# Optimization experiments

Measured on AMD Instinct MI355X. Metric: run time of the kernel, lower is better.

## Reference

```python
import jax, jax.numpy as jnp
import numpy as np

D_MODEL = 1024
NUM_HEAD = 16
D_K = D_MODEL // NUM_HEAD
FFN_D = 4096
EPS = 1e-5


def _layernorm(x, gamma, beta):
    mu = jnp.mean(x, axis=-1, keepdims=True)
    var = jnp.mean(jnp.square(x - mu), axis=-1, keepdims=True)
    return (x - mu) * jax.lax.rsqrt(var + EPS) * gamma + beta


def setup_inputs() -> dict:
    key = jax.random.key(0)
    ks = jax.random.split(key, 16)
    s = 1.0 / np.sqrt(D_MODEL)
    sf = 1.0 / np.sqrt(FFN_D)
    # weights stored as [in, out] (transpose of torch nn.Linear.weight)
    return {
        "x": jax.random.normal(ks[0], (4, 2048, D_MODEL), dtype=jnp.float32),
        "wq": jax.random.uniform(ks[1], (D_MODEL, D_MODEL), jnp.float32, -s, s),
        "bq": jax.random.uniform(ks[2], (D_MODEL,), jnp.float32, -s, s),
        "wk": jax.random.uniform(ks[3], (D_MODEL, D_MODEL), jnp.float32, -s, s),
        "bk": jax.random.uniform(ks[4], (D_MODEL,), jnp.float32, -s, s),
        "wv": jax.random.uniform(ks[5], (D_MODEL, D_MODEL), jnp.float32, -s, s),
        "bv": jax.random.uniform(ks[6], (D_MODEL,), jnp.float32, -s, s),
        "wo": jax.random.uniform(ks[7], (D_MODEL, D_MODEL), jnp.float32, -s, s),
        "bo": jax.random.uniform(ks[8], (D_MODEL,), jnp.float32, -s, s),
        "w1": jax.random.uniform(ks[9], (D_MODEL, FFN_D), jnp.float32, -s, s),
        "b1": jax.random.uniform(ks[10], (FFN_D,), jnp.float32, -s, s),
        "w2": jax.random.uniform(ks[11], (FFN_D, D_MODEL), jnp.float32, -sf, sf),
        "b2": jax.random.uniform(ks[12], (D_MODEL,), jnp.float32, -sf, sf),
        "g1": jnp.ones((D_MODEL,), jnp.float32),
        "be1": jnp.zeros((D_MODEL,), jnp.float32),
        "g2": jnp.ones((D_MODEL,), jnp.float32),
        "be2": jnp.zeros((D_MODEL,), jnp.float32),
    }


def reference(x, wq, bq, wk, bk, wv, bv, wo, bo, w1, b1, w2, b2, g1, be1, g2, be2):
    B, S, _ = x.shape
    resid1 = x
    # project and split heads: [B, H, S, d_k]
    def heads(w, b):
        return (x @ w + b).reshape(B, S, NUM_HEAD, D_K).transpose(0, 2, 1, 3)
    q = heads(wq, bq)
    k = heads(wk, bk)
    v = heads(wv, bv)
    scores = jnp.einsum("bhsd,bhtd->bhst", q, k) / jnp.sqrt(jnp.float32(D_K))
    attn = jax.nn.softmax(scores, axis=-1)
    ctx = jnp.einsum("bhst,bhtd->bhsd", attn, v)
    ctx = ctx.transpose(0, 2, 1, 3).reshape(B, S, D_MODEL)
    attn_out = ctx @ wo + bo
    x1 = _layernorm(resid1 + attn_out, g1, be1)
    ffn = jax.nn.relu(x1 @ w1 + b1) @ w2 + b2
    return _layernorm(x1 + ffn, g2, be2)
```

## Files before the change

### kernel.cpp

```cpp
#include <hip/hip_runtime.h>

typedef unsigned short u16;
typedef __attribute__((ext_vector_type(8))) u16 u16x8;
typedef __attribute__((ext_vector_type(8))) __bf16 bf16x8;
typedef __attribute__((ext_vector_type(4))) float floatx4;
typedef __attribute__((ext_vector_type(16))) float floatx16;
typedef __attribute__((ext_vector_type(4))) unsigned int u32x4;

#define MFMA16(a, b, c) __builtin_amdgcn_mfma_f32_16x16x32_bf16( \
    __builtin_bit_cast(bf16x8, a), __builtin_bit_cast(bf16x8, b), c, 0, 0, 0)
#define MFMA32(a, b, c) __builtin_amdgcn_mfma_f32_32x32x16_bf16( \
    __builtin_bit_cast(bf16x8, a), __builtin_bit_cast(bf16x8, b), c, 0, 0, 0)

#if __has_builtin(__builtin_amdgcn_exp2f)
#define EXP2(x) __builtin_amdgcn_exp2f(x)
#else
#define EXP2(x) exp2f(x)
#endif

__device__ __forceinline__ float bf2f(u16 h) {
  unsigned u = ((unsigned)h) << 16;
  float f;
  __builtin_memcpy(&f, &u, 4);
  return f;
}
__device__ __forceinline__ u16 f2bf(float f) {
  unsigned u;
  __builtin_memcpy(&u, &f, 4);
  u += 0x7fff + ((u >> 16) & 1);
  return (u16)(u >> 16);
}

__device__ __forceinline__ unsigned cvt_pk_bf16(float a, float b) {
  unsigned r;
  asm("v_cvt_pk_bf16_f32 %0, %1, %2" : "=v"(r) : "v"(a), "v"(b));
  return r;
}
__device__ __forceinline__ void pl32_swap(unsigned& a, unsigned& b) {
  asm("v_permlane32_swap_b32 %0, %1" : "+v"(a), "+v"(b));
}

typedef __attribute__((address_space(1))) const unsigned int gas_u32;
typedef __attribute__((address_space(3))) unsigned int las_u32;

__device__ __forceinline__ void gld_lds16(const u16* g, u16* l) {
  __builtin_amdgcn_global_load_lds((gas_u32*)g, (las_u32*)l, 16, 0, 0);
}

__global__ __launch_bounds__(256) void transpose_k(const float* __restrict__ in,
                                                   u16* __restrict__ out, int R, int C) {
  __shared__ u16 tile[64][65];
  int c0 = blockIdx.x * 64, r0 = blockIdx.y * 64;
  int tc = threadIdx.x & 63, tr = threadIdx.x >> 6;
#pragma unroll
  for (int i = 0; i < 16; ++i)
    tile[tr + i * 4][tc] = f2bf(in[(size_t)(r0 + tr + i * 4) * C + c0 + tc]);
  __syncthreads();
#pragma unroll
  for (int i = 0; i < 16; ++i)
    out[(size_t)(c0 + tr + i * 4) * R + r0 + tc] = tile[tc][tr + i * 4];
}

__global__ __launch_bounds__(256) void convert_k(const float* __restrict__ in,
                                                 u16* __restrict__ out) {
  size_t idx = ((size_t)blockIdx.x * 256 + threadIdx.x) * 8;
  floatx4 f0 = *(const floatx4*)(in + idx);
  floatx4 f1 = *(const floatx4*)(in + idx + 4);
  u16x8 o;
#pragma unroll
  for (int e = 0; e < 4; ++e) o[e] = f2bf(f0[e]);
#pragma unroll
  for (int e = 0; e < 4; ++e) o[4 + e] = f2bf(f1[e]);
  *(u16x8*)(out + idx) = o;
}

template <bool C_F32, bool BIAS_ROW>
__global__ __launch_bounds__(256, 2) void gemm_bt(const u16* __restrict__ A,
                                                  const u16* __restrict__ BT,
                                                  const float* __restrict__ bias,
                                                  void* __restrict__ Cv, int M, int N, int K,
                                                  int relu) {
  __shared__ __align__(16) u16 As[2][128 * 64];
  __shared__ __align__(16) u16 Bs[2][128 * 64];
  const int tid = threadIdx.x, lane = tid & 63, wave = tid >> 6;
  const int quad = lane >> 4, l15 = lane & 15;
  const int wr = wave >> 1, wc = wave & 1;
  const int m0 = blockIdx.x * 128, n0 = blockIdx.y * 128;

  floatx4 acc[4][4] = {};

  auto stage = [&](int kt, int buf) {
    int k0 = kt * 64;
#pragma unroll
    for (int p = 0; p < 4; ++p) {
      int chunk = p * 256 + tid;
      int row = chunk >> 3, cc = chunk & 7;
      int gc = cc ^ (row & 7);
      int ldsoff = (p * 256 + wave * 64) * 8;
      gld_lds16(A + (size_t)(m0 + row) * K + k0 + gc * 8, &As[buf][ldsoff]);
      gld_lds16(BT + (size_t)(n0 + row) * K + k0 + gc * 8, &Bs[buf][ldsoff]);
    }
  };

  const int nk = K >> 6;
  stage(0, 0);

  for (int kt = 0; kt < nk; ++kt) {
    const int cur = kt & 1;
    __syncthreads();
    if (kt + 1 < nk) stage(kt + 1, cur ^ 1);

#pragma unroll
    for (int ks = 0; ks < 2; ++ks) {
      u16x8 af[4], bfr[4];
#pragma unroll
      for (int i = 0; i < 4; ++i) {
        int r = wr * 64 + i * 16 + l15;
        af[i] = *(const u16x8*)(&As[cur][r * 64 + (((ks * 4 + quad) ^ (r & 7)) * 8)]);
      }
#pragma unroll
      for (int j = 0; j < 4; ++j) {
        int r = wc * 64 + j * 16 + l15;
        bfr[j] = *(const u16x8*)(&Bs[cur][r * 64 + (((ks * 4 + quad) ^ (r & 7)) * 8)]);
      }
#pragma unroll
      for (int i = 0; i < 4; ++i)
#pragma unroll
        for (int j = 0; j < 4; ++j) acc[i][j] = MFMA16(af[i], bfr[j], acc[i][j]);
    }
  }

#pragma unroll
  for (int j = 0; j < 4; ++j) {
    int col = n0 + wc * 64 + j * 16 + l15;
    float bv = BIAS_ROW ? 0.f : bias[col];
#pragma unroll
    for (int i = 0; i < 4; ++i) {
      int row = m0 + wr * 64 + i * 16 + quad * 4;
#pragma unroll
      for (int r = 0; r < 4; ++r) {
        float v = acc[i][j][r] + (BIAS_ROW ? bias[row + r] : bv);
        if (relu) v = fmaxf(v, 0.f);
        if (C_F32)
          ((float*)Cv)[(size_t)(row + r) * N + col] = v;
        else
          ((u16*)Cv)[(size_t)(row + r) * N + col] = f2bf(v);
      }
    }
  }
}

__global__ __launch_bounds__(256, 4) void attn_k(const u16* __restrict__ Q,
                                                 const u16* __restrict__ Km,
                                                 const u16* __restrict__ Vt,
                                                 u16* __restrict__ O) {
  __shared__ __align__(16) u16 sh[16384];
  const int tid = threadIdx.x, lane = tid & 63, w = tid >> 6;
  const int hi = lane >> 5, l31 = lane & 31;
  const int b = blockIdx.z, h = blockIdx.y, q0 = blockIdx.x * 128;
  const size_t tokbase = (size_t)b * 2048;

#pragma unroll
  for (int p = 0; p < 4; ++p) {
    int chunk = p * 256 + tid, row = chunk >> 3, cc = chunk & 7;
    int gc = cc ^ (row & 7);
    gld_lds16(Q + (tokbase + q0 + row) * 1024 + h * 64 + gc * 8, sh + (p * 256 + w * 64) * 8);
  }
  __syncthreads();
  u16x8 qf[4];
#pragma unroll
  for (int kt = 0; kt < 4; ++kt) {
    int r = w * 32 + l31;
    int sel = (kt * 2 + hi) ^ (r & 7);
    u16x8 t = *(const u16x8*)(sh + r * 64 + sel * 8);
#pragma unroll
    for (int e = 0; e < 8; ++e) t[e] = f2bf(bf2f(t[e]) * 0.18033688011f);
    qf[kt] = t;
  }
  __syncthreads();

  floatx16 oacc0 = {}, oacc1 = {};
  float lsum = 0.f;

  auto stage = [&](int it2, int buf) {
    int t0 = it2 * 64;
#pragma unroll
    for (int p = 0; p < 2; ++p) {
      int chunk = p * 256 + tid;
      int row = chunk >> 3, cc = chunk & 7;
      int gc = cc ^ (row & 7);
      int ldsoff = (p * 256 + w * 64) * 8;
      gld_lds16(Km + (tokbase + t0 + row) * 1024 + h * 64 + gc * 8, sh + buf * 4096 + ldsoff);
      gld_lds16(Vt + ((size_t)(h * 64 + row)) * 8192 + tokbase + t0 + gc * 8,
                sh + 8192 + buf * 4096 + ldsoff);
    }
  };

  stage(0, 0);

  for (int it = 0; it < 32; ++it) {
    const int cur = it & 1;
    __syncthreads();
    if (it + 1 < 32) stage(it + 1, cur ^ 1);
    const u16* kb = sh + cur * 4096;
    const u16* vb = sh + 8192 + cur * 4096;

    u32x4 pf[4];
#pragma unroll
    for (int tt = 0; tt < 2; ++tt) {
      u16x8 ka[4];
#pragma unroll
      for (int kt = 0; kt < 4; ++kt) {
        int r = tt * 32 + l31;
        ka[kt] = *(const u16x8*)(kb + r * 64 + (((kt * 2 + hi) ^ (r & 7)) * 8));
      }
      floatx16 s = {};
      __builtin_amdgcn_s_setprio(1);
#pragma unroll
      for (int kt = 0; kt < 4; ++kt) s = MFMA32(ka[kt], qf[kt], s);
      __builtin_amdgcn_s_setprio(0);

      float p[16];
#pragma unroll
      for (int r = 0; r < 16; ++r) p[r] = EXP2(s[r]);
#pragma unroll
      for (int r = 0; r < 16; ++r) lsum += p[r];
#pragma unroll
      for (int half = 0; half < 2; ++half) {
        unsigned X0 = cvt_pk_bf16(p[half * 8 + 0], p[half * 8 + 1]);
        unsigned X1 = cvt_pk_bf16(p[half * 8 + 2], p[half * 8 + 3]);
        unsigned Y0 = cvt_pk_bf16(p[half * 8 + 4], p[half * 8 + 5]);
        unsigned Y1 = cvt_pk_bf16(p[half * 8 + 6], p[half * 8 + 7]);
        pl32_swap(X0, Y0);
        pl32_swap(X1, Y1);
        u32x4 f;
        f[0] = X0; f[1] = X1; f[2] = Y0; f[3] = Y1;
        pf[tt * 2 + half] = f;
      }
    }

    {
      u16x8 va[4];
#pragma unroll
      for (int kt = 0; kt < 4; ++kt) {
        int r = l31;
        va[kt] = *(const u16x8*)(vb + r * 64 + (((kt * 2 + hi) ^ (r & 7)) * 8));
      }
      __builtin_amdgcn_s_setprio(1);
#pragma unroll
      for (int kt = 0; kt < 4; ++kt)
        oacc0 = MFMA32(va[kt], __builtin_bit_cast(u16x8, pf[kt]), oacc0);
      __builtin_amdgcn_s_setprio(0);
#pragma unroll
      for (int kt = 0; kt < 4; ++kt) {
        int r = 32 + l31;
        va[kt] = *(const u16x8*)(vb + r * 64 + (((kt * 2 + hi) ^ (r & 7)) * 8));
      }
      __builtin_amdgcn_s_setprio(1);
#pragma unroll
      for (int kt = 0; kt < 4; ++kt)
        oacc1 = MFMA32(va[kt], __builtin_bit_cast(u16x8, pf[kt]), oacc1);
      __builtin_amdgcn_s_setprio(0);
    }
  }

  __syncthreads();
  float tot = lsum + __shfl_xor(lsum, 32);
  float inv = 1.0f / fmaxf(tot, 1e-30f);
  const int qrow = w * 32 + l31;
#pragma unroll
  for (int dt = 0; dt < 2; ++dt) {
    const floatx16& oa = dt ? oacc1 : oacc0;
#pragma unroll
    for (int pr = 0; pr < 8; ++pr) {
      float a = oa[2 * pr] * inv, bb = oa[2 * pr + 1] * inv;
      unsigned pkw = (unsigned)f2bf(a) | ((unsigned)f2bf(bb) << 16);
      int d = dt * 32 + (pr & 1) * 2 + (pr >> 1) * 8 + 4 * hi;
      *(unsigned*)(sh + qrow * 72 + d) = pkw;
    }
  }
  __syncthreads();
#pragma unroll
  for (int p2 = 0; p2 < 4; ++p2) {
    int c = p2 * 64 + lane, rl = c >> 3, cc = c & 7;
    u16x8 vv = *(const u16x8*)(sh + (w * 32 + rl) * 72 + cc * 8);
    *(u16x8*)(O + (tokbase + q0 + w * 32 + rl) * 1024 + h * 64 + cc * 8) = vv;
  }
}

template <bool A_F32, bool B_F32, bool OUT_F32>
__global__ __launch_bounds__(256) void ln_k(const void* __restrict__ Av,
                                            const void* __restrict__ Bv,
                                            const float* __restrict__ g,
                                            const float* __restrict__ be,
                                            void* __restrict__ outv) {
  const int lane = threadIdx.x & 63, wave = threadIdx.x >> 6;
  const size_t row = (size_t)blockIdx.x * 4 + wave;
  const size_t base = row * 1024 + lane * 16;
  float v[16];
  if (A_F32) {
    const float* a = (const float*)Av + base;
#pragma unroll
    for (int q = 0; q < 4; ++q) {
      floatx4 t = *(const floatx4*)(a + q * 4);
#pragma unroll
      for (int e = 0; e < 4; ++e) v[q * 4 + e] = t[e];
    }
  } else {
    const u16* a = (const u16*)Av + base;
    u16x8 a0 = *(const u16x8*)a, a1 = *(const u16x8*)(a + 8);
#pragma unroll
    for (int e = 0; e < 8; ++e) {
      v[e] = bf2f(a0[e]);
      v[e + 8] = bf2f(a1[e]);
    }
  }
  if (B_F32) {
    const float* bb = (const float*)Bv + base;
#pragma unroll
    for (int q = 0; q < 4; ++q) {
      floatx4 t = *(const floatx4*)(bb + q * 4);
#pragma unroll
      for (int e = 0; e < 4; ++e) v[q * 4 + e] += t[e];
    }
  } else {
    const u16* bb = (const u16*)Bv + base;
    u16x8 b0 = *(const u16x8*)bb, b1 = *(const u16x8*)(bb + 8);
#pragma unroll
    for (int e = 0; e < 8; ++e) {
      v[e] += bf2f(b0[e]);
      v[e + 8] += bf2f(b1[e]);
    }
  }
  float sum = 0.f, sq = 0.f;
#pragma unroll
  for (int e = 0; e < 16; ++e) {
    sum += v[e];
    sq += v[e] * v[e];
  }
#pragma unroll
  for (int mk = 1; mk < 64; mk <<= 1) {
    sum += __shfl_xor(sum, mk);
    sq += __shfl_xor(sq, mk);
  }
  float mu = sum * (1.f / 1024.f);
  float var = fmaxf(sq * (1.f / 1024.f) - mu * mu, 0.f);
  float rstd = rsqrtf(var + 1e-5f);
  if (OUT_F32) {
    float* o = (float*)outv + base;
#pragma unroll
    for (int q = 0; q < 4; ++q) {
      floatx4 t;
#pragma unroll
      for (int e = 0; e < 4; ++e) {
        int c = lane * 16 + q * 4 + e;
        t[e] = (v[q * 4 + e] - mu) * rstd * g[c] + be[c];
      }
      *(floatx4*)(o + q * 4) = t;
    }
  } else {
    u16x8 o0, o1;
#pragma unroll
    for (int e = 0; e < 8; ++e) {
      int c = lane * 16 + e;
      o0[e] = f2bf((v[e] - mu) * rstd * g[c] + be[c]);
      o1[e] = f2bf((v[e + 8] - mu) * rstd * g[c + 8] + be[c + 8]);
    }
    *(u16x8*)((u16*)outv + base) = o0;
    *(u16x8*)((u16*)outv + base + 8) = o1;
  }
}

extern "C" void kernel_launch(void* const* d_in, const int* in_sizes, int n_in, void* d_out,
                              int out_size, void* d_ws, size_t ws_size, hipStream_t stream) {
  const float* x = (const float*)d_in[0];
  const float* wq = (const float*)d_in[1];
  const float* bq = (const float*)d_in[2];
  const float* wk = (const float*)d_in[3];
  const float* bk = (const float*)d_in[4];
  const float* wv = (const float*)d_in[5];
  const float* bv = (const float*)d_in[6];
  const float* wo = (const float*)d_in[7];
  const float* bo = (const float*)d_in[8];
  const float* w1 = (const float*)d_in[9];
  const float* b1 = (const float*)d_in[10];
  const float* w2 = (const float*)d_in[11];
  const float* b2 = (const float*)d_in[12];
  const float* g1 = (const float*)d_in[13];
  const float* be1 = (const float*)d_in[14];
  const float* g2 = (const float*)d_in[15];
  const float* be2 = (const float*)d_in[16];
  float* out = (float*)d_out;

  u16* W = (u16*)d_ws;
  const size_t M1 = (size_t)1 << 20;
  u16* wqT = W;
  u16* wkT = wqT + M1;
  u16* wvT = wkT + M1;
  u16* woT = wvT + M1;
  u16* w1T = woT + M1;
  u16* w2T = w1T + 4 * M1;
  u16* arena = w2T + 4 * M1;
  const size_t S8M = (size_t)8 << 20;
  u16* xb = arena;
  u16* Qb = arena + S8M;
  u16* Kb = arena + 2 * S8M;
  u16* Vtb = arena + 3 * S8M;
  u16* Cb = arena + 4 * S8M;
  u16* AO = Qb;
  u16* X1 = xb;
  u16* F1 = Qb;

  dim3 blk(256);
  transpose_k<<<dim3(16, 16), blk, 0, stream>>>(wq, wqT, 1024, 1024);
  transpose_k<<<dim3(16, 16), blk, 0, stream>>>(wk, wkT, 1024, 1024);
  transpose_k<<<dim3(16, 16), blk, 0, stream>>>(wv, wvT, 1024, 1024);
  transpose_k<<<dim3(16, 16), blk, 0, stream>>>(wo, woT, 1024, 1024);
  transpose_k<<<dim3(64, 16), blk, 0, stream>>>(w1, w1T, 1024, 4096);
  transpose_k<<<dim3(16, 64), blk, 0, stream>>>(w2, w2T, 4096, 1024);
  convert_k<<<4096, blk, 0, stream>>>(x, xb);

  gemm_bt<false, false><<<dim3(64, 8), blk, 0, stream>>>(xb, wqT, bq, Qb, 8192, 1024, 1024, 0);
  gemm_bt<false, false><<<dim3(64, 8), blk, 0, stream>>>(xb, wkT, bk, Kb, 8192, 1024, 1024, 0);
  gemm_bt<false, true><<<dim3(8, 64), blk, 0, stream>>>(wvT, xb, bv, Vtb, 1024, 8192, 1024, 0);

  attn_k<<<dim3(16, 16, 4), blk, 0, stream>>>(Qb, Kb, Vtb, Cb);

  gemm_bt<false, false><<<dim3(64, 8), blk, 0, stream>>>(Cb, woT, bo, AO, 8192, 1024, 1024, 0);
  ln_k<true, false, false><<<2048, blk, 0, stream>>>(x, AO, g1, be1, X1);

  gemm_bt<false, false><<<dim3(64, 32), blk, 0, stream>>>(X1, w1T, b1, F1, 8192, 4096, 1024, 1);
  gemm_bt<true, false><<<dim3(64, 8), blk, 0, stream>>>(F1, w2T, b2, out, 8192, 1024, 4096, 0);
  ln_k<false, true, true><<<2048, blk, 0, stream>>>(X1, out, g2, be2, out);
}
```

Measured before the change: 528.2 us.

## Deepen GEMM pipeline to five-stage K=32 ring buffer with vmcnt waits

```diff
diff --git a/kernel.cpp b/kernel.cpp
--- a/kernel.cpp
+++ b/kernel.cpp
@@ -80,8 +80,8 @@
                                                   const float* __restrict__ bias,
                                                   void* __restrict__ Cv, int M, int N, int K,
                                                   int relu) {
-  __shared__ __align__(16) u16 As[2][128 * 64];
-  __shared__ __align__(16) u16 Bs[2][128 * 64];
+  __shared__ __align__(16) u16 As[5][128 * 32];
+  __shared__ __align__(16) u16 Bs[5][128 * 32];
   const int tid = threadIdx.x, lane = tid & 63, wave = tid >> 6;
   const int quad = lane >> 4, l15 = lane & 15;
   const int wr = wave >> 1, wc = wave & 1;
@@ -90,44 +90,60 @@
   floatx4 acc[4][4] = {};
 
   auto stage = [&](int kt, int buf) {
-    int k0 = kt * 64;
-#pragma unroll
-    for (int p = 0; p < 4; ++p) {
+    int k0 = kt * 32;
+#pragma unroll
+    for (int p = 0; p < 2; ++p) {
       int chunk = p * 256 + tid;
-      int row = chunk >> 3, cc = chunk & 7;
-      int gc = cc ^ (row & 7);
+      int row = chunk >> 2, cc = chunk & 3;
+      int gc = cc ^ ((row >> 1) & 3);
       int ldsoff = (p * 256 + wave * 64) * 8;
       gld_lds16(A + (size_t)(m0 + row) * K + k0 + gc * 8, &As[buf][ldsoff]);
       gld_lds16(BT + (size_t)(n0 + row) * K + k0 + gc * 8, &Bs[buf][ldsoff]);
     }
   };
 
-  const int nk = K >> 6;
+  const int nk = K >> 5;
   stage(0, 0);
-
+  stage(1, 1);
+  stage(2, 2);
+  stage(3, 3);
+
+  int bc = 0, bn = 4;
   for (int kt = 0; kt < nk; ++kt) {
-    const int cur = kt & 1;
-    __syncthreads();
-    if (kt + 1 < nk) stage(kt + 1, cur ^ 1);
-
-#pragma unroll
-    for (int ks = 0; ks < 2; ++ks) {
-      u16x8 af[4], bfr[4];
-#pragma unroll
-      for (int i = 0; i < 4; ++i) {
-        int r = wr * 64 + i * 16 + l15;
-        af[i] = *(const u16x8*)(&As[cur][r * 64 + (((ks * 4 + quad) ^ (r & 7)) * 8)]);
-      }
-#pragma unroll
-      for (int j = 0; j < 4; ++j) {
-        int r = wc * 64 + j * 16 + l15;
-        bfr[j] = *(const u16x8*)(&Bs[cur][r * 64 + (((ks * 4 + quad) ^ (r & 7)) * 8)]);
-      }
-#pragma unroll
-      for (int i = 0; i < 4; ++i)
-#pragma unroll
-        for (int j = 0; j < 4; ++j) acc[i][j] = MFMA16(af[i], bfr[j], acc[i][j]);
-    }
+    const int rem = nk - 1 - kt;
+    if (rem >= 3)
+      asm volatile("s_waitcnt vmcnt(12)" ::: "memory");
+    else if (rem == 2)
+      asm volatile("s_waitcnt vmcnt(8)" ::: "memory");
+    else if (rem == 1)
+      asm volatile("s_waitcnt vmcnt(4)" ::: "memory");
+    else
+      asm volatile("s_waitcnt vmcnt(0)" ::: "memory");
+    __builtin_amdgcn_sched_barrier(0);
+    __builtin_amdgcn_s_barrier();
+
+    if (kt + 4 < nk) stage(kt + 4, bn);
+
+    u16x8 af[4], bfr[4];
+#pragma unroll
+    for (int i = 0; i < 4; ++i) {
+      int r = wr * 64 + i * 16 + l15;
+      af[i] = *(const u16x8*)(&As[bc][r * 32 + ((quad ^ ((r >> 1) & 3)) * 8)]);
+    }
+#pragma unroll
+    for (int j = 0; j < 4; ++j) {
+      int r = wc * 64 + j * 16 + l15;
+      bfr[j] = *(const u16x8*)(&Bs[bc][r * 32 + ((quad ^ ((r >> 1) & 3)) * 8)]);
+    }
+    __builtin_amdgcn_s_setprio(1);
+#pragma unroll
+    for (int i = 0; i < 4; ++i)
+#pragma unroll
+      for (int j = 0; j < 4; ++j) acc[i][j] = MFMA16(af[i], bfr[j], acc[i][j]);
+    __builtin_amdgcn_s_setprio(0);
+
+    if (++bc == 5) bc = 0;
+    if (++bn == 5) bn = 0;
   }
 
 #pragma unroll
```

Measured after the change: 596.6 us. 13.0% more time.
